# Kernel tuning notes

Measured on AMD Instinct MI355X. Metric: run time of the kernel, lower is better.

## Reference

```python
import jax, jax.numpy as jnp
import numpy as np

N_HEAD = 16
SCALE = True
NEG = 10000.0


def setup_inputs() -> dict:
    key = jax.random.key(0)
    ks = jax.random.split(key, 5)
    B, S, D = 4, 1024, 1024
    x = jax.random.normal(ks[0], (B, S, D), dtype=jnp.float32)
    # GPT-2 Conv1D weights: W has shape [in, out], init ~N(0, 0.02)
    w_attn = jax.random.normal(ks[1], (D, 3 * D), dtype=jnp.float32) * 0.02
    b_attn = jnp.zeros((3 * D,), dtype=jnp.float32)
    w_proj = jax.random.normal(ks[2], (D, D), dtype=jnp.float32) * 0.02
    b_proj = jnp.zeros((D,), dtype=jnp.float32)
    return {"x": x, "w_attn": w_attn, "b_attn": b_attn,
            "w_proj": w_proj, "b_proj": b_proj}


def reference(x, w_attn, b_attn, w_proj, b_proj):
    B, S, D = x.shape
    H = N_HEAD
    hd = D // H
    # c_attn: Conv1D == x @ W + b
    qkv = jnp.einsum('bsd,de->bse', x, w_attn) + b_attn
    q, k, v = jnp.split(qkv, 3, axis=-1)
    # split heads -> [B, H, S, hd]
    q = q.reshape(B, S, H, hd).transpose(0, 2, 1, 3)
    k = k.reshape(B, S, H, hd).transpose(0, 2, 1, 3)
    v = v.reshape(B, S, H, hd).transpose(0, 2, 1, 3)
    # scores [B, H, S, S]
    w = jnp.einsum('bhqd,bhkd->bhqk', q, k)
    if SCALE:
        w = w / jnp.sqrt(jnp.float32(hd))
    # multiplicative causal mask: w*b - 10000*(1-b)
    bmask = jnp.tril(jnp.ones((S, S), dtype=w.dtype))[None, None]
    w = w * bmask - NEG * (1.0 - bmask)
    w = jax.nn.softmax(w, axis=-1)
    # attn_pdrop = 0 -> dropout is identity
    a = jnp.einsum('bhqk,bhkd->bhqd', w, v)
    # merge heads
    a = a.transpose(0, 2, 1, 3).reshape(B, S, D)
    # c_proj; resid_pdrop = 0
    out = jnp.einsum('bsd,de->bse', a, w_proj) + b_proj
    return out
```

## Files before the change

### kernel.cpp

```cpp
#include <hip/hip_runtime.h>
#include <hip/hip_bf16.h>


typedef __bf16 bf16x8 __attribute__((ext_vector_type(8)));
typedef __bf16 bf16x4 __attribute__((ext_vector_type(4)));
typedef float f32x4 __attribute__((ext_vector_type(4)));

__device__ __forceinline__ void load_lds16(const void* g, void* l) {
  __builtin_amdgcn_global_load_lds(
      (const __attribute__((address_space(1))) void*)g,
      (__attribute__((address_space(3))) void*)l, 16, 0, 0);
}

__global__ __launch_bounds__(256) void prep(
    const float* __restrict__ x, const float* __restrict__ w_attn,
    const float* __restrict__ w_proj, __bf16* __restrict__ Xb,
    __bf16* __restrict__ WT_attn, __bf16* __restrict__ WT_proj) {
  __shared__ __bf16 tile[32][33];
  const int blk = blockIdx.x;
  const int tid = threadIdx.x;
  if (blk < 4096) {
    const float* W;
    __bf16* WT;
    int n0, k0, N;
    if (blk < 3072) {
      W = w_attn; WT = WT_attn; N = 3072;
      n0 = (blk % 96) * 32; k0 = (blk / 96) * 32;
    } else {
      W = w_proj; WT = WT_proj; N = 1024;
      const int t = blk - 3072;
      n0 = (t & 31) * 32; k0 = (t >> 5) * 32;
    }
    const int tx = tid & 31, ty = tid >> 5;
#pragma unroll
    for (int j = 0; j < 32; j += 8)
      tile[ty + j][tx] = (__bf16)W[(size_t)(k0 + ty + j) * N + n0 + tx];
    __syncthreads();
#pragma unroll
    for (int j = 0; j < 32; j += 8)
      WT[(size_t)(n0 + ty + j) * 1024 + k0 + tx] = tile[tx][ty + j];
  } else {
    const size_t i = (size_t)(blk - 4096) * 4096 + tid * 16;
    const float4* xp = (const float4*)(x + i);
    float4 a = xp[0], b = xp[1], c = xp[2], d = xp[3];
    bf16x8 o0, o1;
    o0[0] = (__bf16)a.x; o0[1] = (__bf16)a.y; o0[2] = (__bf16)a.z; o0[3] = (__bf16)a.w;
    o0[4] = (__bf16)b.x; o0[5] = (__bf16)b.y; o0[6] = (__bf16)b.z; o0[7] = (__bf16)b.w;
    o1[0] = (__bf16)c.x; o1[1] = (__bf16)c.y; o1[2] = (__bf16)c.z; o1[3] = (__bf16)c.w;
    o1[4] = (__bf16)d.x; o1[5] = (__bf16)d.y; o1[6] = (__bf16)d.z; o1[7] = (__bf16)d.w;
    *(bf16x8*)(Xb + i) = o0;
    *(bf16x8*)(Xb + i + 8) = o1;
  }
}

#define GEMM_CORE(A_, BT_, K_)                                                   \
  __shared__ __bf16 sA[128 * 32];                                               \
  __shared__ __bf16 sB[128 * 32];                                               \
  const int tid = threadIdx.x;                                                  \
  const int lane = tid & 63;                                                    \
  const int wave = tid >> 6;                                                    \
  const int waveM = wave >> 1, waveN = wave & 1;                                \
  const int quad = lane >> 4;                                                   \
  const int l16 = lane & 15;                                                    \
  const int rowBase = blockIdx.y * 128;                                         \
  const int colBase = blockIdx.x * 128;                                         \
  const int rIn = lane >> 2;                                                    \
  const int sIn = lane & 3;                                                     \
  const int gc = sIn ^ (rIn & 3) ^ ((rIn >> 2) & 3);                            \
  const int readSlot = quad ^ (l16 & 3) ^ ((l16 >> 2) & 3);                     \
  f32x4 acc[4][4] = {};                                                         \
  for (int k0 = 0; k0 < K_; k0 += 32) {                                         \
    __syncthreads();                                                            \
    _Pragma("unroll") for (int j = 0; j < 2; ++j) {                             \
      const int rb = wave * 32 + j * 16;                                        \
      load_lds16(&A_[(size_t)(rowBase + rb + rIn) * K_ + k0 + gc * 8],          \
                 &sA[rb * 32]);                                                 \
      load_lds16(&BT_[(size_t)(colBase + rb + rIn) * K_ + k0 + gc * 8],         \
                 &sB[rb * 32]);                                                 \
    }                                                                           \
    __syncthreads();                                                            \
    bf16x8 af[4], bfr[4];                                                       \
    _Pragma("unroll") for (int mt = 0; mt < 4; ++mt)                            \
      af[mt] = *(const bf16x8*)(&sA[(waveM * 64 + mt * 16 + l16) * 32 +         \
                                    readSlot * 8]);                             \
    _Pragma("unroll") for (int nt = 0; nt < 4; ++nt)                            \
      bfr[nt] = *(const bf16x8*)(&sB[(waveN * 64 + nt * 16 + l16) * 32 +        \
                                     readSlot * 8]);                            \
    _Pragma("unroll") for (int mt = 0; mt < 4; ++mt)                            \
    _Pragma("unroll") for (int nt = 0; nt < 4; ++nt)                            \
      acc[mt][nt] = __builtin_amdgcn_mfma_f32_16x16x32_bf16(                    \
          af[mt], bfr[nt], acc[mt][nt], 0, 0, 0);                               \
  }


#define BAR8 asm volatile("s_barrier" ::: "memory")
#define LGKM0 asm volatile("s_waitcnt lgkmcnt(0)" ::: "memory")

#define STG(GMAT, GROW0, K0, LOFF)                                             \
  _Pragma("unroll") for (int i_ = 0; i_ < 2; ++i_)                             \
    load_lds16((GMAT) + (size_t)((GROW0) + i_ * 64 + wave * 8 + srow) * 1024 + \
                   (K0) + schunk * 8,                                          \
               smem8 + (LOFF) + (i_ * 64 + wave * 8) * 64);

#define LDA8(BASE, MH)                                                         \
  _Pragma("unroll") for (int m_ = 0; m_ < 4; ++m_)                             \
  _Pragma("unroll") for (int kk_ = 0; kk_ < 2; ++kk_)                          \
    af[m_][kk_] = *(const bf16x8*)((BASE) + ((MH)*64 + m_ * 16 + l16) * 64 +   \
                                   (((kk_ * 4 + quad) ^ rsw) * 8));

#define LDB8(BASE, NLO)                                                        \
  _Pragma("unroll") for (int n_ = 0; n_ < 2; ++n_)                             \
  _Pragma("unroll") for (int kk_ = 0; kk_ < 2; ++kk_)                          \
    bf[(NLO) + n_][kk_] =                                                      \
        *(const bf16x8*)((BASE) + ((waveN & 1) * 64 + ((NLO) + n_) * 16 +      \
                                   l16) * 64 +                                 \
                         (((kk_ * 4 + quad) ^ rsw) * 8));

#define MFMA_HALF(MH, NLO)                                                     \
  __builtin_amdgcn_s_setprio(1);                                               \
  _Pragma("unroll") for (int m_ = 0; m_ < 4; ++m_)                             \
  _Pragma("unroll") for (int n_ = 0; n_ < 2; ++n_) {                           \
    acc[(MH)*4 + m_][(NLO) + n_] = __builtin_amdgcn_mfma_f32_16x16x32_bf16(    \
        af[m_][0], bf[(NLO) + n_][0], acc[(MH)*4 + m_][(NLO) + n_], 0, 0, 0);  \
    acc[(MH)*4 + m_][(NLO) + n_] = __builtin_amdgcn_mfma_f32_16x16x32_bf16(    \
        af[m_][1], bf[(NLO) + n_][1], acc[(MH)*4 + m_][(NLO) + n_], 0, 0, 0);  \
  }                                                                            \
  __builtin_amdgcn_s_setprio(0);

__global__ __launch_bounds__(512, 2) void gemm_qkv8(
    const __bf16* __restrict__ A, const __bf16* __restrict__ BT,
    const float* __restrict__ bias, __bf16* __restrict__ Qp,
    __bf16* __restrict__ Kp, __bf16* __restrict__ Vt) {
  __shared__ __bf16 smem8[65536];
  const int tid = threadIdx.x;
  const int lane = tid & 63;
  const int wave = tid >> 6;
  const int waveM = wave >> 2;
  const int waveN = wave & 3;
  const int l16 = lane & 15;
  const int quad = lane >> 4;
  const int rsw = l16 & 7;
  const int srow = lane >> 3;
  const int schunk = (lane & 7) ^ srow;

  const int bid = blockIdx.x;
  const int swz = (bid & 7) * 24 + (bid >> 3);
  const int tm = swz / 12, tn = swz - (swz / 12) * 12;
  const int rowBase = tm * 256;
  const int colBase = tn * 256;

  const __bf16* aRd = smem8 + waveM * 8192;
  const __bf16* bRd = smem8 + 16384 + (waveN >> 1) * 8192;

  f32x4 acc[8][4] = {};
  bf16x8 af[4][2], bf[4][2];

  STG(A, rowBase, 0, 0);
  STG(A, rowBase + 128, 0, 8192);
  STG(BT, colBase, 0, 16384);
  STG(BT, colBase + 128, 0, 24576);
  STG(BT, colBase, 64, 32768 + 16384);
  STG(BT, colBase + 128, 64, 32768 + 24576);
  STG(A, rowBase, 64, 32768);
  asm volatile("s_waitcnt vmcnt(6)" ::: "memory");
  BAR8;

  for (int t = 0; t < 8; ++t) {
    const int kO = t * 128 + 64;
    const int kS2 = t * 128 + 128;
    const int kS3 = t * 128 + 192;
    const bool s2 = kS2 < 1024;
    const bool s3 = kS3 < 1024;

    LDA8(aRd, 0);
    LDB8(bRd, 0);
    STG(A, rowBase + 128, kO, 32768 + 8192);
    BAR8; LGKM0;
    MFMA_HALF(0, 0);
    BAR8;

    LDB8(bRd, 2);
    BAR8; LGKM0;
    MFMA_HALF(0, 2);
    BAR8;

    LDA8(aRd, 1);
    if (s2) { STG(BT, colBase, kS2, 16384); }
    BAR8; LGKM0;
    MFMA_HALF(1, 2);
    BAR8;

    if (s2) {
      STG(BT, colBase + 128, kS2, 24576);
      STG(A, rowBase, kS2, 0);
      asm volatile("s_waitcnt vmcnt(6)" ::: "memory");
    } else {
      asm volatile("s_waitcnt vmcnt(0)" ::: "memory");
    }
    BAR8;
    MFMA_HALF(1, 0);
    BAR8;

    LDA8(aRd + 32768, 0);
    LDB8(bRd + 32768, 0);
    if (s2) { STG(A, rowBase + 128, kS2, 8192); }
    BAR8; LGKM0;
    MFMA_HALF(0, 0);
    BAR8;

    LDB8(bRd + 32768, 2);
    BAR8; LGKM0;
    MFMA_HALF(0, 2);
    BAR8;

    LDA8(aRd + 32768, 1);
    if (s3) { STG(BT, colBase, kS3, 32768 + 16384); }
    BAR8; LGKM0;
    MFMA_HALF(1, 2);
    BAR8;

    if (s3) {
      STG(BT, colBase + 128, kS3, 32768 + 24576);
      STG(A, rowBase, kS3, 32768);
    }
    asm volatile("s_waitcnt vmcnt(6)" ::: "memory");
    BAR8;
    MFMA_HALF(1, 0);
    BAR8;
  }

  const int seg = colBase >> 10;
  if (seg == 2) {
#pragma unroll
    for (int mm = 0; mm < 8; ++mm) {
      const int r0 = waveM * 128 + mm * 16 + quad * 4;
#pragma unroll
      for (int n = 0; n < 4; ++n) {
        const int cR = waveN * 64 + n * 16 + l16;
        const float bv = bias[colBase + cR];
        bf16x4 pk;
#pragma unroll
        for (int r = 0; r < 4; ++r) pk[r] = (__bf16)(acc[mm][n][r] + bv);
        *(bf16x4*)(&smem8[cR * 256 + (r0 ^ (l16 << 4))]) = pk;
      }
    }
    __syncthreads();
    const int b_ = rowBase >> 10;
    const int s0 = rowBase & 1023;
    const int hBase = (colBase & 1023) >> 6;
    const int ch = lane & 31;
#pragma unroll
    for (int p = 0; p < 16; ++p) {
      const int c = p * 16 + wave * 2 + (lane >> 5);
      bf16x8 v =
          *(const bf16x8*)(&smem8[c * 256 + ((ch * 8) ^ ((c & 15) << 4))]);
      const int bhd = (b_ * 16 + hBase + (c >> 6)) * 64 + (c & 63);
      *(bf16x8*)(&Vt[(size_t)bhd * 1024 + s0 + ch * 8]) = v;
    }
  } else {
#pragma unroll
    for (int mm = 0; mm < 8; ++mm) {
      const int row0 = rowBase + waveM * 128 + mm * 16 + quad * 4;
#pragma unroll
      for (int n = 0; n < 4; ++n) {
        const int col = colBase + waveN * 64 + n * 16 + l16;
        const float bv = bias[col];
        const int cc = col & 1023;
        __bf16* dst = (seg == 0) ? Qp : Kp;
#pragma unroll
        for (int r = 0; r < 4; ++r) {
          const int row = row0 + r;
          const float v = acc[mm][n][r] + bv;
          const int bh = ((row >> 10) << 4) + (cc >> 6);
          dst[((size_t)bh << 16) + (size_t)(row & 1023) * 64 + (cc & 63)] =
              (__bf16)v;
        }
      }
    }
  }
}

__global__ __launch_bounds__(256) void gemm_out(
    const __bf16* __restrict__ A, const __bf16* __restrict__ BT,
    const float* __restrict__ bias, float* __restrict__ C) {
  GEMM_CORE(A, BT, 1024)
#pragma unroll
  for (int mt = 0; mt < 4; ++mt) {
    const int row = rowBase + waveM * 64 + mt * 16 + quad * 4;
#pragma unroll
    for (int nt = 0; nt < 4; ++nt) {
      const int col = colBase + waveN * 64 + nt * 16 + l16;
      const float bv = bias[col];
#pragma unroll
      for (int r = 0; r < 4; ++r)
        C[(size_t)(row + r) * 1024 + col] = acc[mt][nt][r] + bv;
    }
  }
}

__global__ __launch_bounds__(256) void attn_mfma(
    const __bf16* __restrict__ Qp, const __bf16* __restrict__ Kp,
    const __bf16* __restrict__ VT, __bf16* __restrict__ Aout) {
  __shared__ __bf16 sK[128 * 64];
  __shared__ __bf16 sV[64 * 128];
  __shared__ __bf16 sP[4 * 16 * 128];

  const int tid = threadIdx.x;
  const int lane = tid & 63;
  const int wave = tid >> 6;
  const int quad = lane >> 4;
  const int l16 = lane & 15;
  const int swq = l16 & 7;

  const int bh = blockIdx.x >> 3;
  const int pr = blockIdx.x & 7;
  const int b = bh >> 4, h = bh & 15;
  const int qbA = pr * 64, qbB = (15 - pr) * 64;
  const int ktA_max = pr >> 1, ktB_max = (15 - pr) >> 1;

  const __bf16* Qb = Qp + ((size_t)bh << 16);
  const __bf16* Kb = Kp + ((size_t)bh << 16);
  const __bf16* VTb = VT + (size_t)bh * 64 * 1024;

  bf16x8 qA0A, qA1A, qA0B, qA1B;
  {
    const __bf16* qr = Qb + (size_t)(qbA + wave * 16 + l16) * 64 + quad * 8;
    qA0A = *(const bf16x8*)qr;
    qA1A = *(const bf16x8*)(qr + 32);
    qr = Qb + (size_t)(qbB + wave * 16 + l16) * 64 + quad * 8;
    qA0B = *(const bf16x8*)qr;
    qA1B = *(const bf16x8*)(qr + 32);
  }

  f32x4 OA[4] = {}, OB[4] = {};
  float psA[4] = {0.f, 0.f, 0.f, 0.f}, psB[4] = {0.f, 0.f, 0.f, 0.f};
  __bf16* pw = sP + wave * 2048;

  for (int kt = 0; kt <= ktB_max; ++kt) {
    const int kb = kt * 128;
    __syncthreads();

#pragma unroll
    for (int i = 0; i < 4; ++i) {
      const int rb = wave * 32 + i * 8;
      load_lds16(Kb + (size_t)(kb + rb + (lane >> 3)) * 64 +
                     (((lane & 7) ^ ((lane >> 3) & 7)) << 3),
                 &sK[rb * 64]);
    }
#pragma unroll
    for (int i = 0; i < 4; ++i) {
      const int db = wave * 16 + i * 4;
      const int d = db + (lane >> 4);
      load_lds16(VTb + (size_t)d * 1024 + kb + (((lane & 15) ^ (d & 7)) << 3),
                 &sV[db * 128]);
    }
    __syncthreads();

    {
      float sc[8][4];
#pragma unroll
      for (int n = 0; n < 8; ++n) {
        const int key = n * 16 + l16;
        bf16x8 kB0 = *(const bf16x8*)(&sK[key * 64 + ((quad ^ swq) << 3)]);
        bf16x8 kB1 = *(const bf16x8*)(&sK[key * 64 + (((quad + 4) ^ swq) << 3)]);
        f32x4 c = {};
        c = __builtin_amdgcn_mfma_f32_16x16x32_bf16(qA0B, kB0, c, 0, 0, 0);
        c = __builtin_amdgcn_mfma_f32_16x16x32_bf16(qA1B, kB1, c, 0, 0, 0);
#pragma unroll
        for (int r = 0; r < 4; ++r) sc[n][r] = c[r] * 0.125f;
      }
      if (kt == ktB_max) {
#pragma unroll
        for (int n = 0; n < 8; ++n) {
          const int kg = kb + n * 16 + l16;
#pragma unroll
          for (int r = 0; r < 4; ++r)
            if (kg > qbB + wave * 16 + quad * 4 + r) sc[n][r] = -1.0e30f;
        }
      }
#pragma unroll
      for (int n = 0; n < 8; ++n)
#pragma unroll
        for (int r = 0; r < 4; ++r) {
          float p = __expf(fminf(sc[n][r], 60.0f));
          sc[n][r] = p;
          psB[r] += p;
        }
      {
        const int kb8 = l16 >> 3, lo = l16 & 7;
#pragma unroll
        for (int n = 0; n < 8; ++n) {
          const int chunk = n * 2 + kb8;
#pragma unroll
          for (int r = 0; r < 4; ++r) {
            const int q = quad * 4 + r;
            pw[q * 128 + ((chunk ^ (q & 7)) << 3) + lo] = (__bf16)sc[n][r];
          }
        }
      }
#pragma unroll
      for (int cc = 0; cc < 4; ++cc) {
        bf16x8 pA = *(const bf16x8*)(&pw[l16 * 128 + (((cc * 4 + quad) ^ swq) << 3)]);
#pragma unroll
        for (int nt = 0; nt < 4; ++nt) {
          bf16x8 vB = *(const bf16x8*)(&sV[(nt * 16 + l16) * 128 +
                                           (((cc * 4 + quad) ^ swq) << 3)]);
          OB[nt] = __builtin_amdgcn_mfma_f32_16x16x32_bf16(pA, vB, OB[nt], 0, 0, 0);
        }
      }
    }

    if (kt <= ktA_max) {
      float sc[8][4];
#pragma unroll
      for (int n = 0; n < 8; ++n) {
        const int key = n * 16 + l16;
        bf16x8 kB0 = *(const bf16x8*)(&sK[key * 64 + ((quad ^ swq) << 3)]);
        bf16x8 kB1 = *(const bf16x8*)(&sK[key * 64 + (((quad + 4) ^ swq) << 3)]);
        f32x4 c = {};
        c = __builtin_amdgcn_mfma_f32_16x16x32_bf16(qA0A, kB0, c, 0, 0, 0);
        c = __builtin_amdgcn_mfma_f32_16x16x32_bf16(qA1A, kB1, c, 0, 0, 0);
#pragma unroll
        for (int r = 0; r < 4; ++r) sc[n][r] = c[r] * 0.125f;
      }
      if (kt == ktA_max) {
#pragma unroll
        for (int n = 0; n < 8; ++n) {
          const int kg = kb + n * 16 + l16;
#pragma unroll
          for (int r = 0; r < 4; ++r)
            if (kg > qbA + wave * 16 + quad * 4 + r) sc[n][r] = -1.0e30f;
        }
      }
#pragma unroll
      for (int n = 0; n < 8; ++n)
#pragma unroll
        for (int r = 0; r < 4; ++r) {
          float p = __expf(fminf(sc[n][r], 60.0f));
          sc[n][r] = p;
          psA[r] += p;
        }
      {
        const int kb8 = l16 >> 3, lo = l16 & 7;
#pragma unroll
        for (int n = 0; n < 8; ++n) {
          const int chunk = n * 2 + kb8;
#pragma unroll
          for (int r = 0; r < 4; ++r) {
            const int q = quad * 4 + r;
            pw[q * 128 + ((chunk ^ (q & 7)) << 3) + lo] = (__bf16)sc[n][r];
          }
        }
      }
#pragma unroll
      for (int cc = 0; cc < 4; ++cc) {
        bf16x8 pA = *(const bf16x8*)(&pw[l16 * 128 + (((cc * 4 + quad) ^ swq) << 3)]);
#pragma unroll
        for (int nt = 0; nt < 4; ++nt) {
          bf16x8 vB = *(const bf16x8*)(&sV[(nt * 16 + l16) * 128 +
                                           (((cc * 4 + quad) ^ swq) << 3)]);
          OA[nt] = __builtin_amdgcn_mfma_f32_16x16x32_bf16(pA, vB, OA[nt], 0, 0, 0);
        }
      }
    }
  }

  float invA[4], invB[4];
#pragma unroll
  for (int r = 0; r < 4; ++r) {
    float pa = psA[r], pb = psB[r];
    pa += __shfl_xor(pa, 1); pb += __shfl_xor(pb, 1);
    pa += __shfl_xor(pa, 2); pb += __shfl_xor(pb, 2);
    pa += __shfl_xor(pa, 4); pb += __shfl_xor(pb, 4);
    pa += __shfl_xor(pa, 8); pb += __shfl_xor(pb, 8);
    invA[r] = 1.0f / pa;
    invB[r] = 1.0f / pb;
  }
#pragma unroll
  for (int nt = 0; nt < 4; ++nt) {
#pragma unroll
    for (int r = 0; r < 4; ++r) {
      const int qA = qbA + wave * 16 + quad * 4 + r;
      const int qB = qbB + wave * 16 + quad * 4 + r;
      Aout[((size_t)b * 1024 + qA) * 1024 + h * 64 + nt * 16 + l16] =
          (__bf16)(OA[nt][r] * invA[r]);
      Aout[((size_t)b * 1024 + qB) * 1024 + h * 64 + nt * 16 + l16] =
          (__bf16)(OB[nt][r] * invB[r]);
    }
  }
}

extern "C" void kernel_launch(void* const* d_in, const int* in_sizes, int n_in,
                              void* d_out, int out_size, void* d_ws,
                              size_t ws_size, hipStream_t stream) {
  const float* x      = (const float*)d_in[0];
  const float* w_attn = (const float*)d_in[1];
  const float* b_attn = (const float*)d_in[2];
  const float* w_proj = (const float*)d_in[3];
  const float* b_proj = (const float*)d_in[4];
  float* out = (float*)d_out;

  char* ws = (char*)d_ws;
  __bf16* WT_attn = (__bf16*)(ws);
  __bf16* WT_proj = (__bf16*)(ws + 6291456);
  __bf16* Xb      = (__bf16*)(ws + 8388608);
  __bf16* Qp      = (__bf16*)(ws + 16777216);
  __bf16* Kp      = (__bf16*)(ws + 25165824);
  __bf16* VT      = (__bf16*)(ws + 33554432);
  __bf16* Aattn   = (__bf16*)(ws + 41943040);

  prep<<<5120, 256, 0, stream>>>(x, w_attn, w_proj, Xb, WT_attn, WT_proj);
  gemm_qkv8<<<192, 512, 0, stream>>>(Xb, WT_attn, b_attn, Qp, Kp, VT);
  attn_mfma<<<512, 256, 0, stream>>>(Qp, Kp, VT, Aattn);
  gemm_out<<<dim3(8, 32), 256, 0, stream>>>(Aattn, WT_proj, b_proj, out);
}
```

Before: 171.7 us.

## Multi-buffer LDS staging in output GEMM and attention to overlap loads with MFMA

The output projection GEMM now uses a three-stage LDS ring buffer and prefetches two k-tiles ahead, with vmcnt waits and raw barriers in place of the two __syncthreads per iteration. The attention kernel double-buffers its K and V tiles, issuing the next tile's async loads before computing on the current one. Both kernels wrap their MFMA sections in s_setprio. The aim is to hide global-to-LDS latency behind matrix math, at the cost of more LDS per block, which may lower occupancy. The single-barrier-per-iteration scheme depends on the vmcnt counts being exact to avoid read/write races.

```diff
diff --git a/kernel.cpp b/kernel.cpp
--- a/kernel.cpp
+++ b/kernel.cpp
@@ -11,6 +11,9 @@
       (const __attribute__((address_space(1))) void*)g,
       (__attribute__((address_space(3))) void*)l, 16, 0, 0);
 }
+
+#define BAR8 asm volatile("s_barrier" ::: "memory")
+#define LGKM0 asm volatile("s_waitcnt lgkmcnt(0)" ::: "memory")
 
 __global__ __launch_bounds__(256) void prep(
     const float* __restrict__ x, const float* __restrict__ w_attn,
@@ -53,48 +56,6 @@
   }
 }
 
-#define GEMM_CORE(A_, BT_, K_)                                                   \
-  __shared__ __bf16 sA[128 * 32];                                               \
-  __shared__ __bf16 sB[128 * 32];                                               \
-  const int tid = threadIdx.x;                                                  \
-  const int lane = tid & 63;                                                    \
-  const int wave = tid >> 6;                                                    \
-  const int waveM = wave >> 1, waveN = wave & 1;                                \
-  const int quad = lane >> 4;                                                   \
-  const int l16 = lane & 15;                                                    \
-  const int rowBase = blockIdx.y * 128;                                         \
-  const int colBase = blockIdx.x * 128;                                         \
-  const int rIn = lane >> 2;                                                    \
-  const int sIn = lane & 3;                                                     \
-  const int gc = sIn ^ (rIn & 3) ^ ((rIn >> 2) & 3);                            \
-  const int readSlot = quad ^ (l16 & 3) ^ ((l16 >> 2) & 3);                     \
-  f32x4 acc[4][4] = {};                                                         \
-  for (int k0 = 0; k0 < K_; k0 += 32) {                                         \
-    __syncthreads();                                                            \
-    _Pragma("unroll") for (int j = 0; j < 2; ++j) {                             \
-      const int rb = wave * 32 + j * 16;                                        \
-      load_lds16(&A_[(size_t)(rowBase + rb + rIn) * K_ + k0 + gc * 8],          \
-                 &sA[rb * 32]);                                                 \
-      load_lds16(&BT_[(size_t)(colBase + rb + rIn) * K_ + k0 + gc * 8],         \
-                 &sB[rb * 32]);                                                 \
-    }                                                                           \
-    __syncthreads();                                                            \
-    bf16x8 af[4], bfr[4];                                                       \
-    _Pragma("unroll") for (int mt = 0; mt < 4; ++mt)                            \
-      af[mt] = *(const bf16x8*)(&sA[(waveM * 64 + mt * 16 + l16) * 32 +         \
-                                    readSlot * 8]);                             \
-    _Pragma("unroll") for (int nt = 0; nt < 4; ++nt)                            \
-      bfr[nt] = *(const bf16x8*)(&sB[(waveN * 64 + nt * 16 + l16) * 32 +        \
-                                     readSlot * 8]);                            \
-    _Pragma("unroll") for (int mt = 0; mt < 4; ++mt)                            \
-    _Pragma("unroll") for (int nt = 0; nt < 4; ++nt)                            \
-      acc[mt][nt] = __builtin_amdgcn_mfma_f32_16x16x32_bf16(                    \
-          af[mt], bfr[nt], acc[mt][nt], 0, 0, 0);                               \
-  }
-
-
-#define BAR8 asm volatile("s_barrier" ::: "memory")
-#define LGKM0 asm volatile("s_waitcnt lgkmcnt(0)" ::: "memory")
 
 #define STG(GMAT, GROW0, K0, LOFF)                                             \
   _Pragma("unroll") for (int i_ = 0; i_ < 2; ++i_)                             \
@@ -283,7 +244,68 @@
 __global__ __launch_bounds__(256) void gemm_out(
     const __bf16* __restrict__ A, const __bf16* __restrict__ BT,
     const float* __restrict__ bias, float* __restrict__ C) {
-  GEMM_CORE(A, BT, 1024)
+  __shared__ __bf16 sA[3][128 * 32];
+  __shared__ __bf16 sB[3][128 * 32];
+  const int tid = threadIdx.x;
+  const int lane = tid & 63;
+  const int wave = tid >> 6;
+  const int waveM = wave >> 1, waveN = wave & 1;
+  const int quad = lane >> 4;
+  const int l16 = lane & 15;
+  const int rowBase = blockIdx.y * 128;
+  const int colBase = blockIdx.x * 128;
+  const int rIn = lane >> 2;
+  const int sIn = lane & 3;
+  const int gc = sIn ^ (rIn & 3) ^ ((rIn >> 2) & 3);
+  const int readSlot = quad ^ (l16 & 3) ^ ((l16 >> 2) & 3);
+  f32x4 acc[4][4] = {};
+
+#define GO_STAGE(bi, k0_)                                                      \
+  _Pragma("unroll") for (int j_ = 0; j_ < 2; ++j_) {                           \
+    const int rb = wave * 32 + j_ * 16;                                        \
+    load_lds16(&A[(size_t)(rowBase + rb + rIn) * 1024 + (k0_) + gc * 8],       \
+               &sA[bi][rb * 32]);                                              \
+    load_lds16(&BT[(size_t)(colBase + rb + rIn) * 1024 + (k0_) + gc * 8],      \
+               &sB[bi][rb * 32]);                                              \
+  }
+
+  GO_STAGE(0, 0);
+  GO_STAGE(1, 32);
+  asm volatile("s_waitcnt vmcnt(4)" ::: "memory");
+  BAR8;
+
+#pragma unroll
+  for (int i = 0; i < 32; ++i) {
+    if (i + 2 < 32) { GO_STAGE((i + 2) % 3, (i + 2) * 32); }
+    const __bf16* sAc = sA[i % 3];
+    const __bf16* sBc = sB[i % 3];
+    bf16x8 af[4], bfr[4];
+#pragma unroll
+    for (int mt = 0; mt < 4; ++mt)
+      af[mt] = *(const bf16x8*)(&sAc[(waveM * 64 + mt * 16 + l16) * 32 +
+                                     readSlot * 8]);
+#pragma unroll
+    for (int nt = 0; nt < 4; ++nt)
+      bfr[nt] = *(const bf16x8*)(&sBc[(waveN * 64 + nt * 16 + l16) * 32 +
+                                      readSlot * 8]);
+    __builtin_amdgcn_s_setprio(1);
+#pragma unroll
+    for (int mt = 0; mt < 4; ++mt)
+#pragma unroll
+      for (int nt = 0; nt < 4; ++nt)
+        acc[mt][nt] = __builtin_amdgcn_mfma_f32_16x16x32_bf16(
+            af[mt], bfr[nt], acc[mt][nt], 0, 0, 0);
+    __builtin_amdgcn_s_setprio(0);
+    if (i + 1 < 32) {
+      if (i + 2 < 32) {
+        asm volatile("s_waitcnt vmcnt(4)" ::: "memory");
+      } else {
+        asm volatile("s_waitcnt vmcnt(0)" ::: "memory");
+      }
+      BAR8;
+    }
+  }
+
 #pragma unroll
   for (int mt = 0; mt < 4; ++mt) {
     const int row = rowBase + waveM * 64 + mt * 16 + quad * 4;
@@ -301,8 +323,8 @@
 __global__ __launch_bounds__(256) void attn_mfma(
     const __bf16* __restrict__ Qp, const __bf16* __restrict__ Kp,
     const __bf16* __restrict__ VT, __bf16* __restrict__ Aout) {
-  __shared__ __bf16 sK[128 * 64];
-  __shared__ __bf16 sV[64 * 128];
+  __shared__ __bf16 sK[2][128 * 64];
+  __shared__ __bf16 sV[2][64 * 128];
   __shared__ __bf16 sP[4 * 16 * 128];
 
   const int tid = threadIdx.x;
@@ -336,39 +358,47 @@
   float psA[4] = {0.f, 0.f, 0.f, 0.f}, psB[4] = {0.f, 0.f, 0.f, 0.f};
   __bf16* pw = sP + wave * 2048;
 
+#define ATTN_STAGE(bi, kbase)                                                  \
+  _Pragma("unroll") for (int i_ = 0; i_ < 4; ++i_) {                           \
+    const int rb = wave * 32 + i_ * 8;                                         \
+    load_lds16(Kb + (size_t)((kbase) + rb + (lane >> 3)) * 64 +                \
+                   (((lane & 7) ^ ((lane >> 3) & 7)) << 3),                    \
+               &sK[bi][rb * 64]);                                              \
+  }                                                                            \
+  _Pragma("unroll") for (int i_ = 0; i_ < 4; ++i_) {                           \
+    const int db = wave * 16 + i_ * 4;                                         \
+    const int d = db + (lane >> 4);                                            \
+    load_lds16(VTb + (size_t)d * 1024 + (kbase) +                              \
+                   (((lane & 15) ^ (d & 7)) << 3),                             \
+               &sV[bi][db * 128]);                                             \
+  }
+
+  ATTN_STAGE(0, 0);
+  asm volatile("s_waitcnt vmcnt(0)" ::: "memory");
+  BAR8;
+
   for (int kt = 0; kt <= ktB_max; ++kt) {
     const int kb = kt * 128;
-    __syncthreads();
-
-#pragma unroll
-    for (int i = 0; i < 4; ++i) {
-      const int rb = wave * 32 + i * 8;
-      load_lds16(Kb + (size_t)(kb + rb + (lane >> 3)) * 64 +
-                     (((lane & 7) ^ ((lane >> 3) & 7)) << 3),
-                 &sK[rb * 64]);
-    }
-#pragma unroll
-    for (int i = 0; i < 4; ++i) {
-      const int db = wave * 16 + i * 4;
-      const int d = db + (lane >> 4);
-      load_lds16(VTb + (size_t)d * 1024 + kb + (((lane & 15) ^ (d & 7)) << 3),
-                 &sV[db * 128]);
-    }
-    __syncthreads();
+    const int cur = kt & 1;
+    if (kt < ktB_max) { ATTN_STAGE(cur ^ 1, kb + 128); }
+    const __bf16* skc = sK[cur];
+    const __bf16* svc = sV[cur];
 
     {
       float sc[8][4];
+      __builtin_amdgcn_s_setprio(1);
 #pragma unroll
       for (int n = 0; n < 8; ++n) {
         const int key = n * 16 + l16;
-        bf16x8 kB0 = *(const bf16x8*)(&sK[key * 64 + ((quad ^ swq) << 3)]);
-        bf16x8 kB1 = *(const bf16x8*)(&sK[key * 64 + (((quad + 4) ^ swq) << 3)]);
+        bf16x8 kB0 = *(const bf16x8*)(&skc[key * 64 + ((quad ^ swq) << 3)]);
+        bf16x8 kB1 = *(const bf16x8*)(&skc[key * 64 + (((quad + 4) ^ swq) << 3)]);
         f32x4 c = {};
         c = __builtin_amdgcn_mfma_f32_16x16x32_bf16(qA0B, kB0, c, 0, 0, 0);
         c = __builtin_amdgcn_mfma_f32_16x16x32_bf16(qA1B, kB1, c, 0, 0, 0);
 #pragma unroll
         for (int r = 0; r < 4; ++r) sc[n][r] = c[r] * 0.125f;
       }
+      __builtin_amdgcn_s_setprio(0);
       if (kt == ktB_max) {
 #pragma unroll
         for (int n = 0; n < 8; ++n) {
@@ -398,31 +428,35 @@
           }
         }
       }
+      __builtin_amdgcn_s_setprio(1);
 #pragma unroll
       for (int cc = 0; cc < 4; ++cc) {
         bf16x8 pA = *(const bf16x8*)(&pw[l16 * 128 + (((cc * 4 + quad) ^ swq) << 3)]);
 #pragma unroll
         for (int nt = 0; nt < 4; ++nt) {
-          bf16x8 vB = *(const bf16x8*)(&sV[(nt * 16 + l16) * 128 +
-                                           (((cc * 4 + quad) ^ swq) << 3)]);
+          bf16x8 vB = *(const bf16x8*)(&svc[(nt * 16 + l16) * 128 +
+                                            (((cc * 4 + quad) ^ swq) << 3)]);
           OB[nt] = __builtin_amdgcn_mfma_f32_16x16x32_bf16(pA, vB, OB[nt], 0, 0, 0);
         }
       }
+      __builtin_amdgcn_s_setprio(0);
     }
 
     if (kt <= ktA_max) {
       float sc[8][4];
+      __builtin_amdgcn_s_setprio(1);
 #pragma unroll
       for (int n = 0; n < 8; ++n) {
         const int key = n * 16 + l16;
-        bf16x8 kB0 = *(const bf16x8*)(&sK[key * 64 + ((quad ^ swq) << 3)]);
-        bf16x8 kB1 = *(const bf16x8*)(&sK[key * 64 + (((quad + 4) ^ swq) << 3)]);
+        bf16x8 kB0 = *(const bf16x8*)(&skc[key * 64 + ((quad ^ swq) << 3)]);
+        bf16x8 kB1 = *(const bf16x8*)(&skc[key * 64 + (((quad + 4) ^ swq) << 3)]);
         f32x4 c = {};
         c = __builtin_amdgcn_mfma_f32_16x16x32_bf16(qA0A, kB0, c, 0, 0, 0);
         c = __builtin_amdgcn_mfma_f32_16x16x32_bf16(qA1A, kB1, c, 0, 0, 0);
 #pragma unroll
         for (int r = 0; r < 4; ++r) sc[n][r] = c[r] * 0.125f;
       }
+      __builtin_amdgcn_s_setprio(0);
       if (kt == ktA_max) {
 #pragma unroll
         for (int n = 0; n < 8; ++n) {
@@ -452,16 +486,23 @@
           }
         }
       }
+      __builtin_amdgcn_s_setprio(1);
 #pragma unroll
       for (int cc = 0; cc < 4; ++cc) {
         bf16x8 pA = *(const bf16x8*)(&pw[l16 * 128 + (((cc * 4 + quad) ^ swq) << 3)]);
 #pragma unroll
         for (int nt = 0; nt < 4; ++nt) {
-          bf16x8 vB = *(const bf16x8*)(&sV[(nt * 16 + l16) * 128 +
-                                           (((cc * 4 + quad) ^ swq) << 3)]);
+          bf16x8 vB = *(const bf16x8*)(&svc[(nt * 16 + l16) * 128 +
+                                            (((cc * 4 + quad) ^ swq) << 3)]);
           OA[nt] = __builtin_amdgcn_mfma_f32_16x16x32_bf16(pA, vB, OA[nt], 0, 0, 0);
         }
       }
+      __builtin_amdgcn_s_setprio(0);
+    }
+
+    if (kt < ktB_max) {
+      asm volatile("s_waitcnt vmcnt(0)" ::: "memory");
+      BAR8;
     }
   }
 
```

Result: no change. 170.9 us (-0.5%).
